# Kernel tuning notes

Measured on AMD Instinct MI355X. Metric: run time of the kernel, lower is better.

Reference implementation:

```python
import jax, jax.numpy as jnp
import numpy as np


def setup_inputs() -> dict:
    key = jax.random.key(0)
    ks = jax.random.split(key, 7)
    S, B, D = 8, 32768, 512
    k = 1.0 / np.sqrt(D)
    u = lambda kk, shape: jax.random.uniform(kk, shape, jnp.float32, -k, k)
    return {
        "x": jax.random.normal(ks[0], (S, B, D), jnp.float32),
        "weight_ih": u(ks[1], (3 * D, D)),
        "weight_hh": u(ks[2], (3 * D, D)),
        "bias_ih": u(ks[3], (3 * D,)),
        "bias_hh": u(ks[4], (3 * D,)),
        "w1": u(ks[5], (D, D)),
        "w2": u(ks[6], (D, D)),
    }


def _gru_cell(xi, h, weight_ih, weight_hh, bias_ih, bias_hh):
    # PyTorch GRUCell gate order: r, z, n
    gi = xi @ weight_ih.T + bias_ih  # [B, 3H]
    gh = h @ weight_hh.T + bias_hh   # [B, 3H]
    i_r, i_z, i_n = jnp.split(gi, 3, axis=-1)
    h_r, h_z, h_n = jnp.split(gh, 3, axis=-1)
    r = jax.nn.sigmoid(i_r + h_r)
    z = jax.nn.sigmoid(i_z + h_z)
    n = jnp.tanh(i_n + r * h_n)
    return (1.0 - z) * n + z * h


def reference(x, weight_ih, weight_hh, bias_ih, bias_hh, w1, w2):
    S, B, _ = x.shape
    H = w1.shape[0]

    def step(carry, inp):
        h, x_prev = carry
        xi, i = inp
        h = _gru_cell(xi, h, weight_ih, weight_hh, bias_ih, bias_hh)
        mixed = h @ w1.T + x_prev @ w2.T  # uses x[i-1]
        h = jnp.where(i % 2 == 1, mixed, h)
        return (h, xi), None

    h0 = jnp.zeros((B, H), x.dtype)  # hn=None -> zeros
    (hn, _), _ = jax.lax.scan(step, (h0, x[0]), (x, jnp.arange(S)))
    return hn
```

## Files before the change

### kernel.cpp

```cpp
#include <hip/hip_runtime.h>


#define BDIM 32768
#define DDIM 512
#define BD (BDIM * DDIM)

typedef short bf16x8 __attribute__((ext_vector_type(8)));
typedef float f32x4 __attribute__((ext_vector_type(4)));
typedef unsigned short u16x8 __attribute__((ext_vector_type(8)));

#define AS1 __attribute__((address_space(1)))
#define AS3 __attribute__((address_space(3)))

__device__ __forceinline__ unsigned short f2bf(float f) {
  union { float f; unsigned u; } v; v.f = f;
  return (unsigned short)((v.u + 0x7fffu + ((v.u >> 16) & 1u)) >> 16);
}
__device__ __forceinline__ float bf2f(unsigned short b) {
  union { unsigned u; float f; } v; v.u = (unsigned)b << 16; return v.f;
}
__device__ __forceinline__ float sigmf(float x) { return 1.0f / (1.0f + __expf(-x)); }
__device__ __forceinline__ float tanhf_(float x) { return 1.0f - 2.0f / (__expf(2.0f * x) + 1.0f); }
__device__ __forceinline__ void bar() { asm volatile("s_barrier" ::: "memory"); }
#define LGKM0 asm volatile("s_waitcnt lgkmcnt(0)" ::: "memory")
#define VMCNT(n) asm volatile("s_waitcnt vmcnt(" #n ")" ::: "memory")

__global__ void cvt_bf16_all(const float* __restrict__ in, unsigned short* __restrict__ out) {
  const size_t stride = (size_t)gridDim.x * 256;
  for (size_t i = (size_t)blockIdx.x * 256 + threadIdx.x; i < (size_t)BD; i += stride) {
    const size_t o = i * 8;
    const float4 a = *(const float4*)(in + o);
    const float4 b = *(const float4*)(in + o + 4);
    u16x8 v;
    v[0] = f2bf(a.x); v[1] = f2bf(a.y); v[2] = f2bf(a.z); v[3] = f2bf(a.w);
    v[4] = f2bf(b.x); v[5] = f2bf(b.y); v[6] = f2bf(b.z); v[7] = f2bf(b.w);
    *(u16x8*)(out + o) = v;
  }
}

__global__ void prep_w(const float* __restrict__ wih, const float* __restrict__ whh,
                       const float* __restrict__ w1, const float* __restrict__ w2,
                       unsigned short* __restrict__ Wg, unsigned short* __restrict__ Wm) {
  int i = blockIdx.x * 256 + threadIdx.x;
  if (i < 1536 * 1024) {
    const int j = i >> 10, k = i & 1023;
    Wg[i] = f2bf((k < 512) ? wih[j * 512 + k] : whh[j * 512 + (k - 512)]);
  } else {
    i -= 1536 * 1024;
    const int j = i >> 10, k = i & 1023;
    Wm[i] = f2bf((k < 512) ? w1[j * 512 + k] : w2[j * 512 + (k - 512)]);
  }
}

template <int SET>
__device__ __forceinline__ void mfma16(f32x4 (&acc)[4][4][2], const bf16x8 (&av)[4][2],
                                       const bf16x8 (&bv)[2][2]) {
  __builtin_amdgcn_s_setprio(1);
#pragma unroll
  for (int fm = 0; fm < 4; ++fm)
#pragma unroll
    for (int fn = 0; fn < 2; ++fn)
#pragma unroll
      for (int ks = 0; ks < 2; ++ks)
        acc[SET][fm][fn] = __builtin_amdgcn_mfma_f32_16x16x32_bf16(
            av[fm][ks], bv[fn][ks], acc[SET][fm][fn], 0, 0, 0);
  __builtin_amdgcn_s_setprio(0);
}

__global__ __launch_bounds__(512, 2) void gru_gates(
    const unsigned short* __restrict__ X, const unsigned short* __restrict__ H,
    const unsigned short* __restrict__ Wg, const float* __restrict__ bih,
    const float* __restrict__ bhh, unsigned short* __restrict__ outB) {
  __shared__ char smem[114688];
  const int t = threadIdx.x;
  const int lane = t & 63, wid = t >> 6;
  const int wm = wid >> 1, wn = wid & 1;
  const int xcd = blockIdx.x & 7, ixc = blockIdx.x >> 3;
  const int bm = xcd * 16 + (ixc >> 3);
  const int bn = ixc & 7;

  f32x4 acc[4][4][2];
  const f32x4 z4 = {0.f, 0.f, 0.f, 0.f};
#pragma unroll
  for (int s = 0; s < 4; ++s)
#pragma unroll
    for (int a = 0; a < 4; ++a)
#pragma unroll
      for (int b = 0; b < 2; ++b) acc[s][a][b] = z4;

  const int trow = t >> 3;
  const int tswz = ((t & 7) * 16) ^ ((trow & 7) << 4);
  int asrc[4], bsrc[3];
#pragma unroll
  for (int i = 0; i < 4; ++i) asrc[i] = (bm * 256 + i * 64 + trow) * 1024 + tswz;
#pragma unroll
  for (int g = 0; g < 3; ++g) bsrc[g] = (g * 512 + bn * 64 + trow) * 2048 + tswz;

  const char* Xc = (const char*)X;
  const char* Hc = (const char*)H;
  const char* Wc = (const char*)Wg;

  auto issA = [&](int kt, int i) {
    const char* base = ((kt < 8) ? Xc : Hc) + (kt & 7) * 128 + asrc[i];
    char* dst = smem + (kt & 1) * 57344 + i * 8192 + t * 16;
    __builtin_amdgcn_global_load_lds((const AS1 void*)base, (AS3 void*)dst, 16, 0, 0);
  };
  auto issB = [&](int kt, int g) {
    const char* base = Wc + kt * 128 + bsrc[g];
    char* dst = smem + (kt & 1) * 57344 + 32768 + g * 8192 + t * 16;
    __builtin_amdgcn_global_load_lds((const AS1 void*)base, (AS3 void*)dst, 16, 0, 0);
  };

  bf16x8 av[4][2], bv[2][2];
  auto readA = [&](const char* pa) {
#pragma unroll
    for (int fm = 0; fm < 4; ++fm)
#pragma unroll
      for (int ks = 0; ks < 2; ++ks) {
        const int r = wm * 64 + fm * 16 + (lane & 15);
        const int c = ks * 64 + (lane >> 4) * 16;
        av[fm][ks] = *(const bf16x8*)(pa + r * 128 + (c ^ ((r & 7) << 4)));
      }
  };
  auto readB = [&](const char* pb, int g) {
#pragma unroll
    for (int fn = 0; fn < 2; ++fn)
#pragma unroll
      for (int ks = 0; ks < 2; ++ks) {
        const int r = wn * 32 + fn * 16 + (lane & 15);
        const int c = ks * 64 + (lane >> 4) * 16;
        bv[fn][ks] = *(const bf16x8*)(pb + g * 8192 + r * 128 + (c ^ ((r & 7) << 4)));
      }
  };

  issA(0, 0); issA(0, 1); issA(0, 2); issA(0, 3);
  issB(0, 0); issB(0, 1); issB(0, 2);
  VMCNT(2);
  bar();

#pragma unroll
  for (int half = 0; half < 2; ++half) {
    for (int k8 = 0; k8 < 8; ++k8) {
      const int kt = half * 8 + k8;
      const bool last = (half == 1) && (k8 == 7);
      const char* pa = smem + (kt & 1) * 57344;
      const char* pb = pa + 32768;
      readA(pa);
      readB(pb, 0);
      if (!last) {
        issA(kt + 1, 0); issA(kt + 1, 1); issA(kt + 1, 2);
        VMCNT(4);
      } else {
        VMCNT(1);
      }
      bar(); LGKM0;
      mfma16<0>(acc, av, bv);
      bar();
      readB(pb, 1);
      if (!last) {
        issA(kt + 1, 3); issB(kt + 1, 0);
        VMCNT(5);
      } else {
        VMCNT(0);
      }
      bar(); LGKM0;
      mfma16<1>(acc, av, bv);
      bar();
      readB(pb, 2);
      if (!last) {
        issB(kt + 1, 1); issB(kt + 1, 2);
        VMCNT(2);
      }
      bar(); LGKM0;
      if (half == 0) mfma16<2>(acc, av, bv);
      else           mfma16<3>(acc, av, bv);
      bar();
    }
  }

  const int erow = (lane >> 4) * 4, ecol = lane & 15;
#pragma unroll
  for (int fn = 0; fn < 2; ++fn) {
    const int d = bn * 64 + wn * 32 + fn * 16 + ecol;
    const float br = bih[d] + bhh[d];
    const float bz = bih[512 + d] + bhh[512 + d];
    const float bi = bih[1024 + d];
    const float bh = bhh[1024 + d];
#pragma unroll
    for (int fm = 0; fm < 4; ++fm)
#pragma unroll
      for (int j = 0; j < 4; ++j) {
        const int row = bm * 256 + wm * 64 + fm * 16 + erow + j;
        const size_t off = (size_t)row * 512 + d;
        const float rv = sigmf(acc[0][fm][fn][j] + br);
        const float zv = sigmf(acc[1][fm][fn][j] + bz);
        const float nv = tanhf_(acc[2][fm][fn][j] + bi + rv * (acc[3][fm][fn][j] + bh));
        outB[off] = f2bf((1.0f - zv) * nv + zv * bf2f(H[off]));
      }
  }
}

template <int MH, int NH>
__device__ __forceinline__ void mfmaQ(f32x4 (&acc)[8][4], const bf16x8 (&af)[4][2],
                                      const bf16x8 (&bv)[2][2]) {
  __builtin_amdgcn_s_setprio(1);
#pragma unroll
  for (int fm = 0; fm < 4; ++fm)
#pragma unroll
    for (int fn = 0; fn < 2; ++fn)
#pragma unroll
      for (int ks = 0; ks < 2; ++ks)
        acc[MH * 4 + fm][NH * 2 + fn] = __builtin_amdgcn_mfma_f32_16x16x32_bf16(
            af[fm][ks], bv[fn][ks], acc[MH * 4 + fm][NH * 2 + fn], 0, 0, 0);
  __builtin_amdgcn_s_setprio(0);
}

template <int WF>
__global__ __launch_bounds__(512, 2) void mixed_gemm(
    const unsigned short* __restrict__ Ka, const unsigned short* __restrict__ Kb,
    const unsigned short* __restrict__ Wm,
    unsigned short* __restrict__ outB, float* __restrict__ outF) {
  __shared__ char smem[131072];
  const int t = threadIdx.x;
  const int lane = t & 63, wid = t >> 6;
  const int wm = wid >> 2, wn = wid & 3;
  const int xcd = blockIdx.x & 7, ixc = blockIdx.x >> 3;
  const int bm = xcd * 16 + (ixc >> 1);
  const int bn = ixc & 1;

  f32x4 acc[8][4];
  const f32x4 z4 = {0.f, 0.f, 0.f, 0.f};
#pragma unroll
  for (int a = 0; a < 8; ++a)
#pragma unroll
    for (int b = 0; b < 4; ++b) acc[a][b] = z4;

  const int trow = t >> 3;
  const int tswz = ((t & 7) * 16) ^ ((trow & 7) << 4);
  int asrc[4], bsrc[4];
#pragma unroll
  for (int i = 0; i < 4; ++i) {
    asrc[i] = (bm * 256 + i * 64 + trow) * 1024 + tswz;
    bsrc[i] = (bn * 256 + i * 64 + trow) * 2048 + tswz;
  }
  const char* Kac = (const char*)Ka;
  const char* Kbc = (const char*)Kb;
  const char* Wc = (const char*)Wm;

  auto issA = [&](int kt, int i) {
    const char* base = ((kt < 8) ? Kac : Kbc) + (kt & 7) * 128 + asrc[i];
    char* dst = smem + (kt & 1) * 65536 + i * 8192 + t * 16;
    __builtin_amdgcn_global_load_lds((const AS1 void*)base, (AS3 void*)dst, 16, 0, 0);
  };
  auto issB = [&](int kt, int i) {
    const char* base = Wc + kt * 128 + bsrc[i];
    char* dst = smem + (kt & 1) * 65536 + 32768 + i * 8192 + t * 16;
    __builtin_amdgcn_global_load_lds((const AS1 void*)base, (AS3 void*)dst, 16, 0, 0);
  };

  bf16x8 af[4][2], bf0[2][2], bf1[2][2];
  auto readAm = [&](const char* pa, int mh) {
#pragma unroll
    for (int fm = 0; fm < 4; ++fm)
#pragma unroll
      for (int ks = 0; ks < 2; ++ks) {
        const int r = mh * 128 + wm * 64 + fm * 16 + (lane & 15);
        const int c = ks * 64 + (lane >> 4) * 16;
        af[fm][ks] = *(const bf16x8*)(pa + r * 128 + (c ^ ((r & 7) << 4)));
      }
  };
  auto readBm = [&](const char* pb, int nh, bf16x8 (&bv)[2][2]) {
#pragma unroll
    for (int fn = 0; fn < 2; ++fn)
#pragma unroll
      for (int ks = 0; ks < 2; ++ks) {
        const int r = nh * 128 + wn * 32 + fn * 16 + (lane & 15);
        const int c = ks * 64 + (lane >> 4) * 16;
        bv[fn][ks] = *(const bf16x8*)(pb + r * 128 + (c ^ ((r & 7) << 4)));
      }
  };

  issA(0, 0); issA(0, 1); issB(0, 0); issB(0, 1);
  issB(0, 2); issB(0, 3); issA(0, 2); issA(0, 3);
  VMCNT(4);
  bar();

  for (int kt = 0; kt < 16; ++kt) {
    const bool last = (kt == 15);
    const char* pa = smem + (kt & 1) * 65536;
    const char* pb = pa + 32768;
    readAm(pa, 0);
    readBm(pb, 0, bf0);
    if (!last) { issA(kt + 1, 0); issA(kt + 1, 1); VMCNT(4); }
    else       { VMCNT(2); }
    bar(); LGKM0;
    mfmaQ<0, 0>(acc, af, bf0);
    bar();
    readBm(pb, 1, bf1);
    if (!last) { issB(kt + 1, 0); issB(kt + 1, 1); VMCNT(4); }
    else       { VMCNT(0); }
    bar(); LGKM0;
    mfmaQ<0, 1>(acc, af, bf1);
    bar();
    readAm(pa, 1);
    if (!last) { issB(kt + 1, 2); issB(kt + 1, 3); }
    bar(); LGKM0;
    mfmaQ<1, 0>(acc, af, bf0);
    bar();
    if (!last) { issA(kt + 1, 2); issA(kt + 1, 3); VMCNT(4); }
    bar();
    mfmaQ<1, 1>(acc, af, bf1);
    bar();
  }

  const int erow = (lane >> 4) * 4, ecol = lane & 15;
#pragma unroll
  for (int mh = 0; mh < 2; ++mh)
#pragma unroll
    for (int fm = 0; fm < 4; ++fm)
#pragma unroll
      for (int nh = 0; nh < 2; ++nh)
#pragma unroll
        for (int fn = 0; fn < 2; ++fn) {
          const int col = bn * 256 + nh * 128 + wn * 32 + fn * 16 + ecol;
#pragma unroll
          for (int j = 0; j < 4; ++j) {
            const int row = bm * 256 + mh * 128 + wm * 64 + fm * 16 + erow + j;
            const size_t off = (size_t)row * 512 + col;
            const float v = acc[mh * 4 + fm][nh * 2 + fn][j];
            if constexpr (WF) outF[off] = v;
            else              outB[off] = f2bf(v);
          }
        }
}

extern "C" void kernel_launch(void* const* d_in, const int* in_sizes, int n_in,
                              void* d_out, int out_size, void* d_ws, size_t ws_size,
                              hipStream_t stream) {
  const float* x   = (const float*)d_in[0];
  const float* wih = (const float*)d_in[1];
  const float* whh = (const float*)d_in[2];
  const float* bih = (const float*)d_in[3];
  const float* bhh = (const float*)d_in[4];
  const float* w1  = (const float*)d_in[5];
  const float* w2  = (const float*)d_in[6];

  char* ws = (char*)d_ws;
  const size_t bd2 = (size_t)BD * 2;
  unsigned short* xall  = (unsigned short*)ws;
  unsigned short* hb[2] = {(unsigned short*)(ws + 8 * bd2),
                           (unsigned short*)(ws + 9 * bd2)};
  unsigned short* Wg = (unsigned short*)(ws + 10 * bd2);
  unsigned short* Wm = Wg + 1536 * 1024;

  hipMemsetAsync(hb[0], 0, bd2, stream);
  cvt_bf16_all<<<2048, 256, 0, stream>>>(x, xall);
  prep_w<<<8192, 256, 0, stream>>>(wih, whh, w1, w2, Wg, Wm);

  int hp = 0;
  for (int i = 0; i < 8; ++i) {
    const unsigned short* xi = xall + (size_t)i * BD;
    gru_gates<<<1024, 512, 0, stream>>>(xi, hb[hp], Wg, bih, bhh, hb[hp ^ 1]);
    hp ^= 1;
    if (i & 1) {
      const unsigned short* xprev = xall + (size_t)(i - 1) * BD;
      if (i == 7)
        mixed_gemm<1><<<256, 512, 0, stream>>>(hb[hp], xprev, Wm, nullptr, (float*)d_out);
      else
        mixed_gemm<0><<<256, 512, 0, stream>>>(hb[hp], xprev, Wm, hb[hp ^ 1], nullptr);
      if (i != 7) hp ^= 1;
    }
  }
}
```

Before: 1.275 ms.

## Make GRU gates kernel persistent over four M tiles with cross-tile prefetch

The gru_gates kernel now launches 256 blocks instead of 1024, and each block loops over four M tiles. The first K-tile of the next M tile is prefetched while the current one finishes, so the pipeline is not refilled from scratch. This is meant to cut launch and ramp-up cost and to hide the epilogue behind loads. The explicit lgkmcnt(0) waits after barriers are also removed from both GEMM kernels. That relies on the compiler inserting the LDS waits, and a missing wait would mean a race. Only 256 blocks now run at two per CU, which lowers occupancy and load balance.

```diff
diff --git a/kernel.cpp b/kernel.cpp
--- a/kernel.cpp
+++ b/kernel.cpp
@@ -22,7 +22,6 @@
 __device__ __forceinline__ float sigmf(float x) { return 1.0f / (1.0f + __expf(-x)); }
 __device__ __forceinline__ float tanhf_(float x) { return 1.0f - 2.0f / (__expf(2.0f * x) + 1.0f); }
 __device__ __forceinline__ void bar() { asm volatile("s_barrier" ::: "memory"); }
-#define LGKM0 asm volatile("s_waitcnt lgkmcnt(0)" ::: "memory")
 #define VMCNT(n) asm volatile("s_waitcnt vmcnt(" #n ")" ::: "memory")
 
 __global__ void cvt_bf16_all(const float* __restrict__ in, unsigned short* __restrict__ out) {
@@ -76,8 +75,8 @@
   const int lane = t & 63, wid = t >> 6;
   const int wm = wid >> 1, wn = wid & 1;
   const int xcd = blockIdx.x & 7, ixc = blockIdx.x >> 3;
-  const int bm = xcd * 16 + (ixc >> 3);
   const int bn = ixc & 7;
+  const int mslot = ixc >> 3;
 
   f32x4 acc[4][4][2];
   const f32x4 z4 = {0.f, 0.f, 0.f, 0.f};
@@ -92,7 +91,7 @@
   const int tswz = ((t & 7) * 16) ^ ((trow & 7) << 4);
   int asrc[4], bsrc[3];
 #pragma unroll
-  for (int i = 0; i < 4; ++i) asrc[i] = (bm * 256 + i * 64 + trow) * 1024 + tswz;
+  for (int i = 0; i < 4; ++i) asrc[i] = (i * 64 + trow) * 1024 + tswz;
 #pragma unroll
   for (int g = 0; g < 3; ++g) bsrc[g] = (g * 512 + bn * 64 + trow) * 2048 + tswz;
 
@@ -100,13 +99,16 @@
   const char* Hc = (const char*)H;
   const char* Wc = (const char*)Wg;
 
-  auto issA = [&](int kt, int i) {
-    const char* base = ((kt < 8) ? Xc : Hc) + (kt & 7) * 128 + asrc[i];
+  auto mbase = [&](int q) -> size_t {
+    return (size_t)(xcd * 16 + q * 4 + mslot) << 18;
+  };
+  auto issA = [&](int q, int kt, int i) {
+    const char* base = ((kt < 8) ? Xc : Hc) + mbase(q) + (kt & 7) * 128 + asrc[i];
     char* dst = smem + (kt & 1) * 57344 + i * 8192 + t * 16;
     __builtin_amdgcn_global_load_lds((const AS1 void*)base, (AS3 void*)dst, 16, 0, 0);
   };
   auto issB = [&](int kt, int g) {
-    const char* base = Wc + kt * 128 + bsrc[g];
+    const char* base = Wc + (kt & 15) * 128 + bsrc[g];
     char* dst = smem + (kt & 1) * 57344 + 32768 + g * 8192 + t * 16;
     __builtin_amdgcn_global_load_lds((const AS1 void*)base, (AS3 void*)dst, 16, 0, 0);
   };
@@ -133,70 +135,89 @@
       }
   };
 
-  issA(0, 0); issA(0, 1); issA(0, 2); issA(0, 3);
+  const int erow = (lane >> 4) * 4, ecol = lane & 15;
+
+  issA(0, 0, 0); issA(0, 0, 1); issA(0, 0, 2); issA(0, 0, 3);
   issB(0, 0); issB(0, 1); issB(0, 2);
   VMCNT(2);
   bar();
 
-#pragma unroll
-  for (int half = 0; half < 2; ++half) {
-    for (int k8 = 0; k8 < 8; ++k8) {
-      const int kt = half * 8 + k8;
-      const bool last = (half == 1) && (k8 == 7);
+#pragma unroll 1
+  for (int q = 0; q < 4; ++q) {
+#pragma unroll 2
+    for (int kt = 0; kt < 16; ++kt) {
+      const bool lastT = (kt == 15);
+      const bool lastC = (q == 3);
+      const bool bnd0 = (kt == 0) && (q > 0);
       const char* pa = smem + (kt & 1) * 57344;
       const char* pb = pa + 32768;
       readA(pa);
       readB(pb, 0);
-      if (!last) {
-        issA(kt + 1, 0); issA(kt + 1, 1); issA(kt + 1, 2);
-        VMCNT(4);
+      if (!lastT) {
+        if (!bnd0) { issA(q, kt + 1, 0); issA(q, kt + 1, 1); issA(q, kt + 1, 2); VMCNT(4); }
+      } else if (!lastC) {
+        issA(q + 1, 0, 0); issA(q + 1, 0, 1); issA(q + 1, 0, 2); VMCNT(4);
       } else {
         VMCNT(1);
       }
-      bar(); LGKM0;
+      bar();
       mfma16<0>(acc, av, bv);
       bar();
       readB(pb, 1);
-      if (!last) {
-        issA(kt + 1, 3); issB(kt + 1, 0);
+      if (!lastT) {
+        if (!bnd0) { issA(q, kt + 1, 3); issB(kt + 1, 0); VMCNT(5); }
+      } else if (!lastC) {
+        issA(q + 1, 0, 3); issB(16, 0);
         VMCNT(5);
       } else {
         VMCNT(0);
       }
-      bar(); LGKM0;
+      bar();
       mfma16<1>(acc, av, bv);
       bar();
       readB(pb, 2);
-      if (!last) {
-        issB(kt + 1, 1); issB(kt + 1, 2);
-        VMCNT(2);
-      }
-      bar(); LGKM0;
-      if (half == 0) mfma16<2>(acc, av, bv);
-      else           mfma16<3>(acc, av, bv);
+      if (!lastT) {
+        issB(kt + 1, 1); issB(kt + 1, 2); VMCNT(2);
+      } else if (!lastC) {
+        issB(16, 1); issB(16, 2); VMCNT(2);
+      }
+      bar();
+      if (kt < 8) mfma16<2>(acc, av, bv);
+      else        mfma16<3>(acc, av, bv);
       bar();
     }
-  }
-
-  const int erow = (lane >> 4) * 4, ecol = lane & 15;
-#pragma unroll
-  for (int fn = 0; fn < 2; ++fn) {
-    const int d = bn * 64 + wn * 32 + fn * 16 + ecol;
-    const float br = bih[d] + bhh[d];
-    const float bz = bih[512 + d] + bhh[512 + d];
-    const float bi = bih[1024 + d];
-    const float bh = bhh[1024 + d];
-#pragma unroll
-    for (int fm = 0; fm < 4; ++fm)
-#pragma unroll
-      for (int j = 0; j < 4; ++j) {
-        const int row = bm * 256 + wm * 64 + fm * 16 + erow + j;
-        const size_t off = (size_t)row * 512 + d;
-        const float rv = sigmf(acc[0][fm][fn][j] + br);
-        const float zv = sigmf(acc[1][fm][fn][j] + bz);
-        const float nv = tanhf_(acc[2][fm][fn][j] + bi + rv * (acc[3][fm][fn][j] + bh));
-        outB[off] = f2bf((1.0f - zv) * nv + zv * bf2f(H[off]));
-      }
+
+    const int rbase = (xcd * 16 + q * 4 + mslot) * 256 + wm * 64;
+#pragma unroll
+    for (int fn = 0; fn < 2; ++fn) {
+      const int d = bn * 64 + wn * 32 + fn * 16 + ecol;
+      const float br = bih[d] + bhh[d];
+      const float bz = bih[512 + d] + bhh[512 + d];
+      const float bi = bih[1024 + d];
+      const float bh = bhh[1024 + d];
+#pragma unroll
+      for (int fm = 0; fm < 4; ++fm)
+#pragma unroll
+        for (int j = 0; j < 4; ++j) {
+          const size_t off = (size_t)(rbase + fm * 16 + erow + j) * 512 + d;
+          const float rv = sigmf(acc[0][fm][fn][j] + br);
+          const float zv = sigmf(acc[1][fm][fn][j] + bz);
+          const float nv = tanhf_(acc[2][fm][fn][j] + bi + rv * (acc[3][fm][fn][j] + bh));
+          outB[off] = f2bf((1.0f - zv) * nv + zv * bf2f(H[off]));
+        }
+    }
+
+    if (q < 3) {
+#pragma unroll
+      for (int s = 0; s < 4; ++s)
+#pragma unroll
+        for (int a = 0; a < 4; ++a)
+#pragma unroll
+          for (int b = 0; b < 2; ++b) acc[s][a][b] = z4;
+      VMCNT(0);
+      issA(q + 1, 1, 0); issA(q + 1, 1, 1); issA(q + 1, 1, 2); issA(q + 1, 1, 3);
+      issB(1, 0); issB(1, 1); issB(1, 2);
+    }
   }
 }
 
@@ -293,18 +314,18 @@
     readBm(pb, 0, bf0);
     if (!last) { issA(kt + 1, 0); issA(kt + 1, 1); VMCNT(4); }
     else       { VMCNT(2); }
-    bar(); LGKM0;
+    bar();
     mfmaQ<0, 0>(acc, af, bf0);
     bar();
     readBm(pb, 1, bf1);
     if (!last) { issB(kt + 1, 0); issB(kt + 1, 1); VMCNT(4); }
     else       { VMCNT(0); }
-    bar(); LGKM0;
+    bar();
     mfmaQ<0, 1>(acc, af, bf1);
     bar();
     readAm(pa, 1);
     if (!last) { issB(kt + 1, 2); issB(kt + 1, 3); }
-    bar(); LGKM0;
+    bar();
     mfmaQ<1, 0>(acc, af, bf0);
     bar();
     if (!last) { issA(kt + 1, 2); issA(kt + 1, 3); VMCNT(4); }
@@ -360,7 +381,7 @@
   int hp = 0;
   for (int i = 0; i < 8; ++i) {
     const unsigned short* xi = xall + (size_t)i * BD;
-    gru_gates<<<1024, 512, 0, stream>>>(xi, hb[hp], Wg, bih, bhh, hb[hp ^ 1]);
+    gru_gates<<<256, 512, 0, stream>>>(xi, hb[hp], Wg, bih, bhh, hb[hp ^ 1]);
     hp ^= 1;
     if (i & 1) {
       const unsigned short* xprev = xall + (size_t)(i - 1) * BD;
```

New measurement: 1.516 ms. 1.19x slower.

## Hoist input-side GRU and mixing GEMMs out of recurrence into batched precompute

Applied to the files above, without the earlier changes.

The input projections x@W_ih^T for all steps, and x_prev@W2^T for the mixing steps, are now computed up front in large batched GEMM launches. The sequential per-step kernels then only multiply h by W_hh or W1, halving their K dimension. Step 0 with h=0 becomes an elementwise kernel, and the zero memset is dropped. The cost is extra workspace and global traffic for the bf16 precomputed gate buffers, which are read back in each step's epilogue. The explicit LDS waitcnt after barriers is also removed.

```diff
diff --git a/kernel.cpp b/kernel.cpp
--- a/kernel.cpp
+++ b/kernel.cpp
@@ -22,7 +22,6 @@
 __device__ __forceinline__ float sigmf(float x) { return 1.0f / (1.0f + __expf(-x)); }
 __device__ __forceinline__ float tanhf_(float x) { return 1.0f - 2.0f / (__expf(2.0f * x) + 1.0f); }
 __device__ __forceinline__ void bar() { asm volatile("s_barrier" ::: "memory"); }
-#define LGKM0 asm volatile("s_waitcnt lgkmcnt(0)" ::: "memory")
 #define VMCNT(n) asm volatile("s_waitcnt vmcnt(" #n ")" ::: "memory")
 
 __global__ void cvt_bf16_all(const float* __restrict__ in, unsigned short* __restrict__ out) {
@@ -53,7 +52,7 @@
 }
 
 template <int SET>
-__device__ __forceinline__ void mfma16(f32x4 (&acc)[4][4][2], const bf16x8 (&av)[4][2],
+__device__ __forceinline__ void mfma16(f32x4 (&acc)[3][4][2], const bf16x8 (&av)[4][2],
                                        const bf16x8 (&bv)[2][2]) {
   __builtin_amdgcn_s_setprio(1);
 #pragma unroll
@@ -67,48 +66,61 @@
   __builtin_amdgcn_s_setprio(0);
 }
 
-__global__ __launch_bounds__(512, 2) void gru_gates(
-    const unsigned short* __restrict__ X, const unsigned short* __restrict__ H,
-    const unsigned short* __restrict__ Wg, const float* __restrict__ bih,
-    const float* __restrict__ bhh, unsigned short* __restrict__ outB) {
-  __shared__ char smem[114688];
+template <int MODE>
+__global__ __launch_bounds__(256, 2) void gru3(
+    const unsigned short* __restrict__ A, const unsigned short* __restrict__ Wg,
+    const float* __restrict__ bih, const float* __restrict__ bhh,
+    const unsigned short* __restrict__ GX, unsigned short* __restrict__ out) {
+  __shared__ char smem[81920];
   const int t = threadIdx.x;
   const int lane = t & 63, wid = t >> 6;
   const int wm = wid >> 1, wn = wid & 1;
-  const int xcd = blockIdx.x & 7, ixc = blockIdx.x >> 3;
-  const int bm = xcd * 16 + (ixc >> 3);
+
+  int bidx = blockIdx.x;
+  int s = 0;
+  if constexpr (MODE == 0) { s = bidx >> 11; bidx &= 2047; }
+  const int xcd = bidx & 7, ixc = bidx >> 3;
+  const int bm = xcd * 32 + (ixc >> 3);
   const int bn = ixc & 7;
-
-  f32x4 acc[4][4][2];
+  constexpr int KOFF = (MODE == 0) ? 0 : 8;
+
+  f32x4 acc[3][4][2];
   const f32x4 z4 = {0.f, 0.f, 0.f, 0.f};
 #pragma unroll
-  for (int s = 0; s < 4; ++s)
+  for (int g = 0; g < 3; ++g)
 #pragma unroll
     for (int a = 0; a < 4; ++a)
 #pragma unroll
-      for (int b = 0; b < 2; ++b) acc[s][a][b] = z4;
+      for (int b = 0; b < 2; ++b) acc[g][a][b] = z4;
 
   const int trow = t >> 3;
-  const int tswz = ((t & 7) * 16) ^ ((trow & 7) << 4);
-  int asrc[4], bsrc[3];
-#pragma unroll
-  for (int i = 0; i < 4; ++i) asrc[i] = (bm * 256 + i * 64 + trow) * 1024 + tswz;
-#pragma unroll
-  for (int g = 0; g < 3; ++g) bsrc[g] = (g * 512 + bn * 64 + trow) * 2048 + tswz;
-
-  const char* Xc = (const char*)X;
-  const char* Hc = (const char*)H;
-  const char* Wc = (const char*)Wg;
+  const int tcs = (t & 7) * 16;
+  int asrc[4], bsrc[3][2];
+#pragma unroll
+  for (int i = 0; i < 4; ++i) {
+    const int r = i * 32 + trow;
+    asrc[i] = (bm * 128 + r) * 1024 + (tcs ^ ((r & 7) << 4));
+  }
+#pragma unroll
+  for (int g = 0; g < 3; ++g)
+#pragma unroll
+    for (int j = 0; j < 2; ++j) {
+      const int r = j * 32 + trow;
+      bsrc[g][j] = (g * 512 + bn * 64 + r) * 2048 + (tcs ^ ((r & 7) << 4));
+    }
+
+  const char* Ac = (const char*)A + (MODE == 0 ? (size_t)s * BD * 2 : 0);
+  const char* Wc = (const char*)Wg + KOFF * 128;
 
   auto issA = [&](int kt, int i) {
-    const char* base = ((kt < 8) ? Xc : Hc) + (kt & 7) * 128 + asrc[i];
-    char* dst = smem + (kt & 1) * 57344 + i * 8192 + t * 16;
-    __builtin_amdgcn_global_load_lds((const AS1 void*)base, (AS3 void*)dst, 16, 0, 0);
-  };
-  auto issB = [&](int kt, int g) {
-    const char* base = Wc + kt * 128 + bsrc[g];
-    char* dst = smem + (kt & 1) * 57344 + 32768 + g * 8192 + t * 16;
-    __builtin_amdgcn_global_load_lds((const AS1 void*)base, (AS3 void*)dst, 16, 0, 0);
+    __builtin_amdgcn_global_load_lds((const AS1 void*)(Ac + kt * 128 + asrc[i]),
+                                     (AS3 void*)(smem + (kt & 1) * 40960 + i * 4096 + t * 16),
+                                     16, 0, 0);
+  };
+  auto issB = [&](int kt, int g, int j) {
+    __builtin_amdgcn_global_load_lds(
+        (const AS1 void*)(Wc + kt * 128 + bsrc[g][j]),
+        (AS3 void*)(smem + (kt & 1) * 40960 + 16384 + g * 8192 + j * 4096 + t * 16), 16, 0, 0);
   };
 
   bf16x8 av[4][2], bv[2][2];
@@ -134,73 +146,94 @@
   };
 
   issA(0, 0); issA(0, 1); issA(0, 2); issA(0, 3);
-  issB(0, 0); issB(0, 1); issB(0, 2);
-  VMCNT(2);
+  issB(0, 0, 0); issB(0, 0, 1); issB(0, 1, 0); issB(0, 1, 1); issB(0, 2, 0); issB(0, 2, 1);
+  VMCNT(4);
   bar();
 
 #pragma unroll
-  for (int half = 0; half < 2; ++half) {
-    for (int k8 = 0; k8 < 8; ++k8) {
-      const int kt = half * 8 + k8;
-      const bool last = (half == 1) && (k8 == 7);
-      const char* pa = smem + (kt & 1) * 57344;
-      const char* pb = pa + 32768;
-      readA(pa);
-      readB(pb, 0);
-      if (!last) {
-        issA(kt + 1, 0); issA(kt + 1, 1); issA(kt + 1, 2);
-        VMCNT(4);
-      } else {
-        VMCNT(1);
-      }
-      bar(); LGKM0;
-      mfma16<0>(acc, av, bv);
-      bar();
-      readB(pb, 1);
-      if (!last) {
-        issA(kt + 1, 3); issB(kt + 1, 0);
-        VMCNT(5);
-      } else {
-        VMCNT(0);
-      }
-      bar(); LGKM0;
-      mfma16<1>(acc, av, bv);
-      bar();
-      readB(pb, 2);
-      if (!last) {
-        issB(kt + 1, 1); issB(kt + 1, 2);
-        VMCNT(2);
-      }
-      bar(); LGKM0;
-      if (half == 0) mfma16<2>(acc, av, bv);
-      else           mfma16<3>(acc, av, bv);
-      bar();
+  for (int kt = 0; kt < 8; ++kt) {
+    const bool last = (kt == 7);
+    const char* pa = smem + (kt & 1) * 40960;
+    const char* pb = pa + 16384;
+    readA(pa);
+    readB(pb, 0);
+    if (!last) { issA(kt + 1, 0); issA(kt + 1, 1); issA(kt + 1, 2); issA(kt + 1, 3); VMCNT(6); }
+    else       { VMCNT(2); }
+    bar();
+    mfma16<0>(acc, av, bv);
+    bar();
+    readB(pb, 1);
+    if (!last) { issB(kt + 1, 0, 0); issB(kt + 1, 0, 1); issB(kt + 1, 1, 0); VMCNT(7); }
+    else       { VMCNT(0); }
+    bar();
+    mfma16<1>(acc, av, bv);
+    bar();
+    readB(pb, 2);
+    if (!last) { issB(kt + 1, 1, 1); issB(kt + 1, 2, 0); issB(kt + 1, 2, 1); VMCNT(4); }
+    bar();
+    mfma16<2>(acc, av, bv);
+    bar();
+  }
+
+  const int erow = (lane >> 4) * 4, ecol = lane & 15;
+  if constexpr (MODE == 0) {
+    unsigned short* gout = out + (size_t)s * 3 * (size_t)BD;
+#pragma unroll
+    for (int fn = 0; fn < 2; ++fn) {
+      const int d = bn * 64 + wn * 32 + fn * 16 + ecol;
+      const float b0 = bih[d], b1 = bih[512 + d], b2 = bih[1024 + d];
+#pragma unroll
+      for (int fm = 0; fm < 4; ++fm)
+#pragma unroll
+        for (int j = 0; j < 4; ++j) {
+          const size_t row = (size_t)(bm * 128 + wm * 64 + fm * 16 + erow + j);
+          gout[row * 1536 + d]        = f2bf(acc[0][fm][fn][j] + b0);
+          gout[row * 1536 + 512 + d]  = f2bf(acc[1][fm][fn][j] + b1);
+          gout[row * 1536 + 1024 + d] = f2bf(acc[2][fm][fn][j] + b2);
+        }
     }
-  }
-
-  const int erow = (lane >> 4) * 4, ecol = lane & 15;
-#pragma unroll
-  for (int fn = 0; fn < 2; ++fn) {
-    const int d = bn * 64 + wn * 32 + fn * 16 + ecol;
-    const float br = bih[d] + bhh[d];
-    const float bz = bih[512 + d] + bhh[512 + d];
-    const float bi = bih[1024 + d];
-    const float bh = bhh[1024 + d];
-#pragma unroll
-    for (int fm = 0; fm < 4; ++fm)
-#pragma unroll
-      for (int j = 0; j < 4; ++j) {
-        const int row = bm * 256 + wm * 64 + fm * 16 + erow + j;
-        const size_t off = (size_t)row * 512 + d;
-        const float rv = sigmf(acc[0][fm][fn][j] + br);
-        const float zv = sigmf(acc[1][fm][fn][j] + bz);
-        const float nv = tanhf_(acc[2][fm][fn][j] + bi + rv * (acc[3][fm][fn][j] + bh));
-        outB[off] = f2bf((1.0f - zv) * nv + zv * bf2f(H[off]));
-      }
-  }
-}
-
-template <int MH, int NH>
+  } else {
+#pragma unroll
+    for (int fn = 0; fn < 2; ++fn) {
+      const int d = bn * 64 + wn * 32 + fn * 16 + ecol;
+      const float bhr = bhh[d], bhz = bhh[512 + d], bhn = bhh[1024 + d];
+#pragma unroll
+      for (int fm = 0; fm < 4; ++fm)
+#pragma unroll
+        for (int j = 0; j < 4; ++j) {
+          const size_t row = (size_t)(bm * 128 + wm * 64 + fm * 16 + erow + j);
+          const size_t off = row * 512 + d;
+          const float rv = sigmf(bf2f(GX[row * 1536 + d]) + acc[0][fm][fn][j] + bhr);
+          const float zv = sigmf(bf2f(GX[row * 1536 + 512 + d]) + acc[1][fm][fn][j] + bhz);
+          const float nv = tanhf_(bf2f(GX[row * 1536 + 1024 + d]) +
+                                  rv * (acc[2][fm][fn][j] + bhn));
+          out[off] = f2bf((1.0f - zv) * nv + zv * bf2f(A[off]));
+        }
+    }
+  }
+}
+
+__global__ void step0(const unsigned short* __restrict__ GX0, const float* __restrict__ bhh,
+                      unsigned short* __restrict__ h1) {
+  const int idx = blockIdx.x * 256 + threadIdx.x;
+  const size_t row = idx >> 6;
+  const int d0 = (idx & 63) * 8;
+  const u16x8 gr = *(const u16x8*)&GX0[row * 1536 + d0];
+  const u16x8 gz = *(const u16x8*)&GX0[row * 1536 + 512 + d0];
+  const u16x8 gn = *(const u16x8*)&GX0[row * 1536 + 1024 + d0];
+  u16x8 o;
+#pragma unroll
+  for (int e = 0; e < 8; ++e) {
+    const int d = d0 + e;
+    const float rv = sigmf(bf2f(gr[e]) + bhh[d]);
+    const float zv = sigmf(bf2f(gz[e]) + bhh[512 + d]);
+    const float nv = tanhf_(bf2f(gn[e]) + rv * bhh[1024 + d]);
+    o[e] = f2bf((1.0f - zv) * nv);
+  }
+  *(u16x8*)&h1[row * 512 + d0] = o;
+}
+
+template <int MH_, int NH_>
 __device__ __forceinline__ void mfmaQ(f32x4 (&acc)[8][4], const bf16x8 (&af)[4][2],
                                       const bf16x8 (&bv)[2][2]) {
   __builtin_amdgcn_s_setprio(1);
@@ -210,23 +243,27 @@
     for (int fn = 0; fn < 2; ++fn)
 #pragma unroll
       for (int ks = 0; ks < 2; ++ks)
-        acc[MH * 4 + fm][NH * 2 + fn] = __builtin_amdgcn_mfma_f32_16x16x32_bf16(
-            af[fm][ks], bv[fn][ks], acc[MH * 4 + fm][NH * 2 + fn], 0, 0, 0);
+        acc[MH_ * 4 + fm][NH_ * 2 + fn] = __builtin_amdgcn_mfma_f32_16x16x32_bf16(
+            af[fm][ks], bv[fn][ks], acc[MH_ * 4 + fm][NH_ * 2 + fn], 0, 0, 0);
   __builtin_amdgcn_s_setprio(0);
 }
 
-template <int WF>
-__global__ __launch_bounds__(512, 2) void mixed_gemm(
-    const unsigned short* __restrict__ Ka, const unsigned short* __restrict__ Kb,
-    const unsigned short* __restrict__ Wm,
+template <int MODE>
+__global__ __launch_bounds__(512, 2) void mixq(
+    const unsigned short* __restrict__ A, const unsigned short* __restrict__ Wm,
+    const unsigned short* __restrict__ MXin,
     unsigned short* __restrict__ outB, float* __restrict__ outF) {
   __shared__ char smem[131072];
   const int t = threadIdx.x;
   const int lane = t & 63, wid = t >> 6;
   const int wm = wid >> 2, wn = wid & 3;
-  const int xcd = blockIdx.x & 7, ixc = blockIdx.x >> 3;
+  int bidx = blockIdx.x;
+  int s2 = 0;
+  if constexpr (MODE == 0) { s2 = bidx >> 8; bidx &= 255; }
+  const int xcd = bidx & 7, ixc = bidx >> 3;
   const int bm = xcd * 16 + (ixc >> 1);
   const int bn = ixc & 1;
+  constexpr int KOFF = (MODE == 0) ? 8 : 0;
 
   f32x4 acc[8][4];
   const f32x4 z4 = {0.f, 0.f, 0.f, 0.f};
@@ -236,26 +273,26 @@
     for (int b = 0; b < 4; ++b) acc[a][b] = z4;
 
   const int trow = t >> 3;
-  const int tswz = ((t & 7) * 16) ^ ((trow & 7) << 4);
+  const int tcs = (t & 7) * 16;
   int asrc[4], bsrc[4];
 #pragma unroll
   for (int i = 0; i < 4; ++i) {
-    asrc[i] = (bm * 256 + i * 64 + trow) * 1024 + tswz;
-    bsrc[i] = (bn * 256 + i * 64 + trow) * 2048 + tswz;
-  }
-  const char* Kac = (const char*)Ka;
-  const char* Kbc = (const char*)Kb;
-  const char* Wc = (const char*)Wm;
+    const int r = i * 64 + trow;
+    asrc[i] = (bm * 256 + r) * 1024 + (tcs ^ ((r & 7) << 4));
+    bsrc[i] = (bn * 256 + r) * 2048 + (tcs ^ ((r & 7) << 4));
+  }
+  const char* Ac = (const char*)A + (MODE == 0 ? (size_t)s2 * 2 * (size_t)BD * 2 : 0);
+  const char* Wc = (const char*)Wm + KOFF * 128;
 
   auto issA = [&](int kt, int i) {
-    const char* base = ((kt < 8) ? Kac : Kbc) + (kt & 7) * 128 + asrc[i];
-    char* dst = smem + (kt & 1) * 65536 + i * 8192 + t * 16;
-    __builtin_amdgcn_global_load_lds((const AS1 void*)base, (AS3 void*)dst, 16, 0, 0);
+    __builtin_amdgcn_global_load_lds((const AS1 void*)(Ac + kt * 128 + asrc[i]),
+                                     (AS3 void*)(smem + (kt & 1) * 65536 + i * 8192 + t * 16),
+                                     16, 0, 0);
   };
   auto issB = [&](int kt, int i) {
-    const char* base = Wc + kt * 128 + bsrc[i];
-    char* dst = smem + (kt & 1) * 65536 + 32768 + i * 8192 + t * 16;
-    __builtin_amdgcn_global_load_lds((const AS1 void*)base, (AS3 void*)dst, 16, 0, 0);
+    __builtin_amdgcn_global_load_lds(
+        (const AS1 void*)(Wc + kt * 128 + bsrc[i]),
+        (AS3 void*)(smem + (kt & 1) * 65536 + 32768 + i * 8192 + t * 16), 16, 0, 0);
   };
 
   bf16x8 af[4][2], bf0[2][2], bf1[2][2];
@@ -285,26 +322,27 @@
   VMCNT(4);
   bar();
 
-  for (int kt = 0; kt < 16; ++kt) {
-    const bool last = (kt == 15);
+#pragma unroll
+  for (int kt = 0; kt < 8; ++kt) {
+    const bool last = (kt == 7);
     const char* pa = smem + (kt & 1) * 65536;
     const char* pb = pa + 32768;
     readAm(pa, 0);
     readBm(pb, 0, bf0);
     if (!last) { issA(kt + 1, 0); issA(kt + 1, 1); VMCNT(4); }
     else       { VMCNT(2); }
-    bar(); LGKM0;
+    bar();
     mfmaQ<0, 0>(acc, af, bf0);
     bar();
     readBm(pb, 1, bf1);
     if (!last) { issB(kt + 1, 0); issB(kt + 1, 1); VMCNT(4); }
     else       { VMCNT(0); }
-    bar(); LGKM0;
+    bar();
     mfmaQ<0, 1>(acc, af, bf1);
     bar();
     readAm(pa, 1);
     if (!last) { issB(kt + 1, 2); issB(kt + 1, 3); }
-    bar(); LGKM0;
+    bar();
     mfmaQ<1, 0>(acc, af, bf0);
     bar();
     if (!last) { issA(kt + 1, 2); issA(kt + 1, 3); VMCNT(4); }
@@ -314,6 +352,7 @@
   }
 
   const int erow = (lane >> 4) * 4, ecol = lane & 15;
+  unsigned short* oB = (MODE == 0) ? outB + (size_t)s2 * (size_t)BD : outB;
 #pragma unroll
   for (int mh = 0; mh < 2; ++mh)
 #pragma unroll
@@ -325,11 +364,12 @@
           const int col = bn * 256 + nh * 128 + wn * 32 + fn * 16 + ecol;
 #pragma unroll
           for (int j = 0; j < 4; ++j) {
-            const int row = bm * 256 + mh * 128 + wm * 64 + fm * 16 + erow + j;
-            const size_t off = (size_t)row * 512 + col;
-            const float v = acc[mh * 4 + fm][nh * 2 + fn][j];
-            if constexpr (WF) outF[off] = v;
-            else              outB[off] = f2bf(v);
+            const size_t row = (size_t)(bm * 256 + mh * 128 + wm * 64 + fm * 16 + erow + j);
+            const size_t off = row * 512 + col;
+            float v = acc[mh * 4 + fm][nh * 2 + fn][j];
+            if constexpr (MODE != 0) v += bf2f(MXin[off]);
+            if constexpr (MODE == 2) outF[off] = v;
+            else                     oB[off] = f2bf(v);
           }
         }
 }
@@ -350,25 +390,32 @@
   unsigned short* xall  = (unsigned short*)ws;
   unsigned short* hb[2] = {(unsigned short*)(ws + 8 * bd2),
                            (unsigned short*)(ws + 9 * bd2)};
-  unsigned short* Wg = (unsigned short*)(ws + 10 * bd2);
-  unsigned short* Wm = Wg + 1536 * 1024;
-
-  hipMemsetAsync(hb[0], 0, bd2, stream);
+  unsigned short* MX    = (unsigned short*)(ws + 10 * bd2);
+  unsigned short* GXb   = (unsigned short*)(ws + 14 * bd2);
+  unsigned short* Wg    = (unsigned short*)(ws + 38 * bd2);
+  unsigned short* Wm    = Wg + 1536 * 1024;
+
   cvt_bf16_all<<<2048, 256, 0, stream>>>(x, xall);
   prep_w<<<8192, 256, 0, stream>>>(wih, whh, w1, w2, Wg, Wm);
 
+  gru3<0><<<16384, 256, 0, stream>>>(xall, Wg, bih, bhh, nullptr, GXb);
+  mixq<0><<<1024, 512, 0, stream>>>(xall, Wm, nullptr, MX, nullptr);
+
+  step0<<<8192, 256, 0, stream>>>(GXb, bhh, hb[0]);
+
   int hp = 0;
-  for (int i = 0; i < 8; ++i) {
-    const unsigned short* xi = xall + (size_t)i * BD;
-    gru_gates<<<1024, 512, 0, stream>>>(xi, hb[hp], Wg, bih, bhh, hb[hp ^ 1]);
+  for (int i = 1; i < 8; ++i) {
+    const unsigned short* GXi = GXb + (size_t)i * 3 * (size_t)BD;
+    gru3<1><<<2048, 256, 0, stream>>>(hb[hp], Wg, bih, bhh, GXi, hb[hp ^ 1]);
     hp ^= 1;
     if (i & 1) {
-      const unsigned short* xprev = xall + (size_t)(i - 1) * BD;
-      if (i == 7)
-        mixed_gemm<1><<<256, 512, 0, stream>>>(hb[hp], xprev, Wm, nullptr, (float*)d_out);
-      else
-        mixed_gemm<0><<<256, 512, 0, stream>>>(hb[hp], xprev, Wm, hb[hp ^ 1], nullptr);
-      if (i != 7) hp ^= 1;
+      const unsigned short* mx = MX + (size_t)((i - 1) / 2) * (size_t)BD;
+      if (i == 7) {
+        mixq<2><<<256, 512, 0, stream>>>(hb[hp], Wm, mx, nullptr, (float*)d_out);
+      } else {
+        mixq<1><<<256, 512, 0, stream>>>(hb[hp], Wm, mx, hb[hp ^ 1], nullptr);
+        hp ^= 1;
+      }
     }
   }
 }
```

After: 1.622 ms. +27.2%, slower.

## Restructure GRU gate GEMM with triple-buffered A tiles and per-phase gate MFMAs

Applied to the files above, without the earlier changes.

Reworks the gru_gates main loop so A tiles use a three-slot LDS ring, prefetched two k-steps ahead, while B uses a double buffer. Each k-step is now two phases that compute all three gate column groups at once, with fewer barriers. The accumulator layout and B fragment mapping are reorganised to fit, and explicit lgkmcnt waits are removed in both GEMM kernels. The cost is more LDS (144KB), which can hurt occupancy with two blocks per CU. Dropping the lgkmcnt waits leaves the LDS-read ordering to the compiler.

```diff
diff --git a/kernel.cpp b/kernel.cpp
--- a/kernel.cpp
+++ b/kernel.cpp
@@ -22,7 +22,6 @@
 __device__ __forceinline__ float sigmf(float x) { return 1.0f / (1.0f + __expf(-x)); }
 __device__ __forceinline__ float tanhf_(float x) { return 1.0f - 2.0f / (__expf(2.0f * x) + 1.0f); }
 __device__ __forceinline__ void bar() { asm volatile("s_barrier" ::: "memory"); }
-#define LGKM0 asm volatile("s_waitcnt lgkmcnt(0)" ::: "memory")
 #define VMCNT(n) asm volatile("s_waitcnt vmcnt(" #n ")" ::: "memory")
 
 __global__ void cvt_bf16_all(const float* __restrict__ in, unsigned short* __restrict__ out) {
@@ -52,26 +51,11 @@
   }
 }
 
-template <int SET>
-__device__ __forceinline__ void mfma16(f32x4 (&acc)[4][4][2], const bf16x8 (&av)[4][2],
-                                       const bf16x8 (&bv)[2][2]) {
-  __builtin_amdgcn_s_setprio(1);
-#pragma unroll
-  for (int fm = 0; fm < 4; ++fm)
-#pragma unroll
-    for (int fn = 0; fn < 2; ++fn)
-#pragma unroll
-      for (int ks = 0; ks < 2; ++ks)
-        acc[SET][fm][fn] = __builtin_amdgcn_mfma_f32_16x16x32_bf16(
-            av[fm][ks], bv[fn][ks], acc[SET][fm][fn], 0, 0, 0);
-  __builtin_amdgcn_s_setprio(0);
-}
-
 __global__ __launch_bounds__(512, 2) void gru_gates(
     const unsigned short* __restrict__ X, const unsigned short* __restrict__ H,
     const unsigned short* __restrict__ Wg, const float* __restrict__ bih,
     const float* __restrict__ bhh, unsigned short* __restrict__ outB) {
-  __shared__ char smem[114688];
+  __shared__ char smem[147456];
   const int t = threadIdx.x;
   const int lane = t & 63, wid = t >> 6;
   const int wm = wid >> 1, wn = wid & 1;
@@ -79,14 +63,12 @@
   const int bm = xcd * 16 + (ixc >> 3);
   const int bn = ixc & 7;
 
-  f32x4 acc[4][4][2];
+  f32x4 acc[4][8];
   const f32x4 z4 = {0.f, 0.f, 0.f, 0.f};
 #pragma unroll
-  for (int s = 0; s < 4; ++s)
-#pragma unroll
-    for (int a = 0; a < 4; ++a)
-#pragma unroll
-      for (int b = 0; b < 2; ++b) acc[s][a][b] = z4;
+  for (int a = 0; a < 4; ++a)
+#pragma unroll
+    for (int b = 0; b < 8; ++b) acc[a][b] = z4;
 
   const int trow = t >> 3;
   const int tswz = ((t & 7) * 16) ^ ((trow & 7) << 4);
@@ -100,88 +82,72 @@
   const char* Hc = (const char*)H;
   const char* Wc = (const char*)Wg;
 
-  auto issA = [&](int kt, int i) {
-    const char* base = ((kt < 8) ? Xc : Hc) + (kt & 7) * 128 + asrc[i];
-    char* dst = smem + (kt & 1) * 57344 + i * 8192 + t * 16;
-    __builtin_amdgcn_global_load_lds((const AS1 void*)base, (AS3 void*)dst, 16, 0, 0);
-  };
-  auto issB = [&](int kt, int g) {
-    const char* base = Wc + kt * 128 + bsrc[g];
-    char* dst = smem + (kt & 1) * 57344 + 32768 + g * 8192 + t * 16;
-    __builtin_amdgcn_global_load_lds((const AS1 void*)base, (AS3 void*)dst, 16, 0, 0);
-  };
-
-  bf16x8 av[4][2], bv[2][2];
-  auto readA = [&](const char* pa) {
-#pragma unroll
-    for (int fm = 0; fm < 4; ++fm)
-#pragma unroll
-      for (int ks = 0; ks < 2; ++ks) {
-        const int r = wm * 64 + fm * 16 + (lane & 15);
-        const int c = ks * 64 + (lane >> 4) * 16;
-        av[fm][ks] = *(const bf16x8*)(pa + r * 128 + (c ^ ((r & 7) << 4)));
-      }
-  };
-  auto readB = [&](const char* pb, int g) {
-#pragma unroll
-    for (int fn = 0; fn < 2; ++fn)
-#pragma unroll
-      for (int ks = 0; ks < 2; ++ks) {
-        const int r = wn * 32 + fn * 16 + (lane & 15);
-        const int c = ks * 64 + (lane >> 4) * 16;
-        bv[fn][ks] = *(const bf16x8*)(pb + g * 8192 + r * 128 + (c ^ ((r & 7) << 4)));
-      }
+  auto issA = [&](int tt, int i) {
+    const char* base = ((tt < 8) ? Xc : Hc) + (tt & 7) * 128 + asrc[i];
+    __builtin_amdgcn_global_load_lds(
+        (const AS1 void*)base,
+        (AS3 void*)(smem + (tt % 3) * 32768 + i * 8192 + t * 16), 16, 0, 0);
+  };
+  auto issB = [&](int tt, int g) {
+    const char* base = Wc + tt * 128 + bsrc[g];
+    __builtin_amdgcn_global_load_lds(
+        (const AS1 void*)base,
+        (AS3 void*)(smem + 98304 + (tt & 1) * 24576 + g * 8192 + t * 16), 16, 0, 0);
   };
 
   issA(0, 0); issA(0, 1); issA(0, 2); issA(0, 3);
   issB(0, 0); issB(0, 1); issB(0, 2);
-  VMCNT(2);
+  issA(1, 0); issA(1, 1); issA(1, 2); issA(1, 3);
+  VMCNT(4);
   bar();
 
 #pragma unroll
-  for (int half = 0; half < 2; ++half) {
-    for (int k8 = 0; k8 < 8; ++k8) {
-      const int kt = half * 8 + k8;
-      const bool last = (half == 1) && (k8 == 7);
-      const char* pa = smem + (kt & 1) * 57344;
-      const char* pb = pa + 32768;
-      readA(pa);
-      readB(pb, 0);
-      if (!last) {
-        issA(kt + 1, 0); issA(kt + 1, 1); issA(kt + 1, 2);
-        VMCNT(4);
+  for (int kt = 0; kt < 16; ++kt) {
+    const char* pa = smem + (kt % 3) * 32768;
+    const char* pb = smem + 98304 + (kt & 1) * 24576;
+#pragma unroll
+    for (int ph = 0; ph < 2; ++ph) {
+      bf16x8 av[4], bv[6];
+      const int ksb = ph * 64 + (lane >> 4) * 16;
+#pragma unroll
+      for (int fm = 0; fm < 4; ++fm) {
+        const int r = wm * 64 + fm * 16 + (lane & 15);
+        av[fm] = *(const bf16x8*)(pa + r * 128 + (ksb ^ ((r & 7) << 4)));
+      }
+#pragma unroll
+      for (int fn = 0; fn < 6; ++fn) {
+        const int c = (fn >> 1) * 64 + (fn & 1) * 32 + wn * 16 + (lane & 15);
+        bv[fn] = *(const bf16x8*)(pb + c * 128 + (ksb ^ ((c & 7) << 4)));
+      }
+      if (ph == 0) {
+        if (kt < 15) { issB(kt + 1, 0); issB(kt + 1, 1); issB(kt + 1, 2); }
       } else {
-        VMCNT(1);
-      }
-      bar(); LGKM0;
-      mfma16<0>(acc, av, bv);
+        if (kt < 14) {
+          issA(kt + 2, 0); issA(kt + 2, 1); issA(kt + 2, 2); issA(kt + 2, 3);
+          VMCNT(4);
+        } else if (kt == 14) {
+          VMCNT(0);
+        }
+      }
       bar();
-      readB(pb, 1);
-      if (!last) {
-        issA(kt + 1, 3); issB(kt + 1, 0);
-        VMCNT(5);
-      } else {
-        VMCNT(0);
-      }
-      bar(); LGKM0;
-      mfma16<1>(acc, av, bv);
-      bar();
-      readB(pb, 2);
-      if (!last) {
-        issB(kt + 1, 1); issB(kt + 1, 2);
-        VMCNT(2);
-      }
-      bar(); LGKM0;
-      if (half == 0) mfma16<2>(acc, av, bv);
-      else           mfma16<3>(acc, av, bv);
+      __builtin_amdgcn_s_setprio(1);
+#pragma unroll
+      for (int fn = 0; fn < 6; ++fn) {
+        const int ai = (fn < 4 || kt < 8) ? fn : fn + 2;
+#pragma unroll
+        for (int fm = 0; fm < 4; ++fm)
+          acc[fm][ai] = __builtin_amdgcn_mfma_f32_16x16x32_bf16(av[fm], bv[fn],
+                                                               acc[fm][ai], 0, 0, 0);
+      }
+      __builtin_amdgcn_s_setprio(0);
       bar();
     }
   }
 
   const int erow = (lane >> 4) * 4, ecol = lane & 15;
 #pragma unroll
-  for (int fn = 0; fn < 2; ++fn) {
-    const int d = bn * 64 + wn * 32 + fn * 16 + ecol;
+  for (int e = 0; e < 2; ++e) {
+    const int d = bn * 64 + e * 32 + wn * 16 + ecol;
     const float br = bih[d] + bhh[d];
     const float bz = bih[512 + d] + bhh[512 + d];
     const float bi = bih[1024 + d];
@@ -192,9 +158,9 @@
       for (int j = 0; j < 4; ++j) {
         const int row = bm * 256 + wm * 64 + fm * 16 + erow + j;
         const size_t off = (size_t)row * 512 + d;
-        const float rv = sigmf(acc[0][fm][fn][j] + br);
-        const float zv = sigmf(acc[1][fm][fn][j] + bz);
-        const float nv = tanhf_(acc[2][fm][fn][j] + bi + rv * (acc[3][fm][fn][j] + bh));
+        const float rv = sigmf(acc[fm][0 + e][j] + br);
+        const float zv = sigmf(acc[fm][2 + e][j] + bz);
+        const float nv = tanhf_(acc[fm][4 + e][j] + bi + rv * (acc[fm][6 + e][j] + bh));
         outB[off] = f2bf((1.0f - zv) * nv + zv * bf2f(H[off]));
       }
   }
@@ -249,13 +215,15 @@
 
   auto issA = [&](int kt, int i) {
     const char* base = ((kt < 8) ? Kac : Kbc) + (kt & 7) * 128 + asrc[i];
-    char* dst = smem + (kt & 1) * 65536 + i * 8192 + t * 16;
-    __builtin_amdgcn_global_load_lds((const AS1 void*)base, (AS3 void*)dst, 16, 0, 0);
+    __builtin_amdgcn_global_load_lds(
+        (const AS1 void*)base,
+        (AS3 void*)(smem + (kt & 1) * 65536 + i * 8192 + t * 16), 16, 0, 0);
   };
   auto issB = [&](int kt, int i) {
     const char* base = Wc + kt * 128 + bsrc[i];
-    char* dst = smem + (kt & 1) * 65536 + 32768 + i * 8192 + t * 16;
-    __builtin_amdgcn_global_load_lds((const AS1 void*)base, (AS3 void*)dst, 16, 0, 0);
+    __builtin_amdgcn_global_load_lds(
+        (const AS1 void*)base,
+        (AS3 void*)(smem + (kt & 1) * 65536 + 32768 + i * 8192 + t * 16), 16, 0, 0);
   };
 
   bf16x8 af[4][2], bf0[2][2], bf1[2][2];
@@ -293,18 +261,18 @@
     readBm(pb, 0, bf0);
     if (!last) { issA(kt + 1, 0); issA(kt + 1, 1); VMCNT(4); }
     else       { VMCNT(2); }
-    bar(); LGKM0;
+    bar();
     mfmaQ<0, 0>(acc, af, bf0);
     bar();
     readBm(pb, 1, bf1);
     if (!last) { issB(kt + 1, 0); issB(kt + 1, 1); VMCNT(4); }
     else       { VMCNT(0); }
-    bar(); LGKM0;
+    bar();
     mfmaQ<0, 1>(acc, af, bf1);
     bar();
     readAm(pa, 1);
     if (!last) { issB(kt + 1, 2); issB(kt + 1, 3); }
-    bar(); LGKM0;
+    bar();
     mfmaQ<1, 0>(acc, af, bf0);
     bar();
     if (!last) { issA(kt + 1, 2); issA(kt + 1, 3); VMCNT(4); }
```

After: 1.229 ms. 3.6% less time.
